# Kernel tuning notes

Hardware: AMD Instinct MI355X
Metric: run time of the kernel (lower is better)

Reference implementation:

```python
import jax, jax.numpy as jnp
import numpy as np

UNITS = 1024
NEG_INF = -10000.0


def setup_inputs() -> dict:
    key = jax.random.key(0)
    ks = jax.random.split(key, 5)
    B, S, D = 8, 2048, 1024
    scale = 0.02  # truncated-normal stddev in original init
    x = jax.random.normal(ks[0], (B, S, D), dtype=jnp.float32)
    mask = jax.random.randint(ks[1], (B, S), 0, 2, dtype=jnp.int32)
    Wq = jax.random.normal(ks[2], (D, UNITS), dtype=jnp.float32) * scale
    Wk = jax.random.normal(ks[3], (D, UNITS), dtype=jnp.float32) * scale
    Wv = jax.random.normal(ks[4], (D, UNITS), dtype=jnp.float32) * scale
    bq = jnp.zeros((UNITS,), jnp.float32)
    bk = jnp.zeros((UNITS,), jnp.float32)
    bv = jnp.zeros((UNITS,), jnp.float32)
    return {"x": x, "mask": mask, "Wq": Wq, "bq": bq, "Wk": Wk, "bk": bk, "Wv": Wv, "bv": bv}


def reference(x, mask, Wq, bq, Wk, bk, Wv, bv):
    # Q/K/V projections: [B,S,D] @ [D,U] -> [B,S,U]
    q = jnp.einsum('bsd,du->bsu', x, Wq) + bq
    k = jnp.einsum('bsd,du->bsu', x, Wk) + bk
    v = jnp.einsum('bsd,du->bsu', x, Wv) + bv
    # scaled dot-product scores: [B,S,S]
    scores = jnp.einsum('bqu,bku->bqk', q, k) / jnp.sqrt(jnp.float32(UNITS))
    m = mask.astype(jnp.float32)
    attn_mask = jnp.einsum('bq,bk->bqk', m, m)  # outer-product padding mask
    scores = scores + (1.0 - attn_mask) * NEG_INF
    probs = jax.nn.softmax(scores, axis=-1)
    # dropout is inactive at inference (training=None/False in Keras)
    context = jnp.einsum('bqk,bku->bqu', probs, v)
    return context
```

## Files before the change

### kernel.cpp

```cpp
#include <hip/hip_runtime.h>
#include <stdint.h>

typedef unsigned short u16;
typedef __bf16 bf16x8 __attribute__((ext_vector_type(8)));
typedef float f32x4 __attribute__((ext_vector_type(4)));
typedef unsigned short u16x8 __attribute__((ext_vector_type(8)));
typedef unsigned short u16x4 __attribute__((ext_vector_type(4)));

#define B_BATCH 8
#define S_LEN   2048
#define D_DIM   1024
#define U_DIM   1024

#define BK 64
#define HALF_U16  16384
#define TILE_U16  32768
#define LDS_U16   65536

__device__ __forceinline__ float bf2f(u16 h) {
    union { unsigned u; float f; } c; c.u = ((unsigned)h) << 16; return c.f;
}
__device__ __forceinline__ u16 f2bf(float f) {
    union { float f; unsigned u; } c; c.f = f;
    unsigned r = c.u + 0x7fffu + ((c.u >> 16) & 1u);
    return (u16)(r >> 16);
}

__device__ __forceinline__ void cp16(u16* lds, const u16* g) {
    __builtin_amdgcn_global_load_lds((__attribute__((address_space(1))) void*)g,
                                     (__attribute__((address_space(3))) void*)lds,
                                     16, 0, 0);
}

__device__ __forceinline__ void barrier_raw() { asm volatile("s_barrier" ::: "memory"); }

__device__ __forceinline__ void stage4(u16* __restrict__ dst, const u16* __restrict__ src,
                                       int ld, int row0, int kc, int tid) {
    #pragma unroll
    for (int s = 0; s < 4; ++s) {
        const int c = tid + 512 * s;
        const int r = c >> 3;
        const int q = (c & 7) ^ (r & 7);
        cp16(dst + c * 8, src + (long long)(row0 + r) * ld + kc + q * 8);
    }
}

__device__ __forceinline__ void ldsA8(bf16x8* a, const u16* __restrict__ T,
                                      int rbase, int lm, int lq, int sw) {
    #pragma unroll
    for (int i = 0; i < 4; ++i)
        #pragma unroll
        for (int ks = 0; ks < 2; ++ks)
            a[i * 2 + ks] = *(const bf16x8*)(T + (rbase + i * 16 + lm) * BK + (((ks * 4 + lq) ^ sw) * 8));
}
__device__ __forceinline__ void ldsB4(bf16x8* b, const u16* __restrict__ T,
                                      int rbase, int lm, int lq, int sw) {
    #pragma unroll
    for (int j = 0; j < 2; ++j)
        #pragma unroll
        for (int ks = 0; ks < 2; ++ks)
            b[j * 2 + ks] = *(const bf16x8*)(T + (rbase + j * 16 + lm) * BK + (((ks * 4 + lq) ^ sw) * 8));
}

template<int I0, int J0>
__device__ __forceinline__ void mmaq(f32x4 (*acc)[4], const bf16x8* a, const bf16x8* b) {
    __builtin_amdgcn_s_setprio(1);
    #pragma unroll
    for (int i = 0; i < 4; ++i)
        #pragma unroll
        for (int j = 0; j < 2; ++j)
            #pragma unroll
            for (int ks = 0; ks < 2; ++ks)
                acc[I0 + i][J0 + j] = __builtin_amdgcn_mfma_f32_16x16x32_bf16(
                    a[i * 2 + ks], b[j * 2 + ks], acc[I0 + i][J0 + j], 0, 0, 0);
    __builtin_amdgcn_s_setprio(0);
    __builtin_amdgcn_sched_barrier(0);
}

__device__ __forceinline__ void gemm256(
    const u16* __restrict__ A, int lda,
    const u16* __restrict__ Bt, int ldb,
    int m0, int n0, int K,
    u16* lds, int tid, f32x4 (*acc)[4])
{
    const int lane = tid & 63;
    const int wid  = tid >> 6;
    const int wmh  = (wid >> 2) * 128;
    const int wnh  = (wid & 3) * 64;
    const int lm   = lane & 15;
    const int lq   = lane >> 4;
    const int sw   = lm & 7;

    stage4(lds,            A,  lda, m0, 0, tid);
    stage4(lds + HALF_U16, Bt, ldb, n0, 0, tid);
    asm volatile("s_waitcnt vmcnt(0)" ::: "memory");
    barrier_raw();

    const int NT = K >> 6;
    int buf = 0;
    for (int kt = 0; kt < NT; ++kt) {
        const u16* As  = lds + buf * TILE_U16;
        const u16* Bs  = As + HALF_U16;
        u16* Asn = lds + (buf ^ 1) * TILE_U16;
        u16* Bsn = Asn + HALF_U16;
        const int kn = (kt + 1) << 6;
        const bool pre = (kt + 1) < NT;
        bf16x8 a[8], b[4];

        ldsA8(a, As, wmh, lm, lq, sw);
        ldsB4(b, Bs, wnh, lm, lq, sw);
        if (pre) stage4(Asn, A, lda, m0, kn, tid);
        barrier_raw();
        mmaq<0, 0>(acc, a, b);
        barrier_raw();

        ldsB4(b, Bs, wnh + 32, lm, lq, sw);
        if (pre) stage4(Bsn, Bt, ldb, n0, kn, tid);
        barrier_raw();
        mmaq<0, 2>(acc, a, b);
        barrier_raw();

        ldsA8(a, As, wmh + 64, lm, lq, sw);
        barrier_raw();
        mmaq<4, 2>(acc, a, b);
        barrier_raw();

        ldsB4(b, Bs, wnh, lm, lq, sw);
        if (pre) asm volatile("s_waitcnt vmcnt(0)" ::: "memory");
        barrier_raw();
        mmaq<4, 0>(acc, a, b);
        barrier_raw();

        buf ^= 1;
    }
}

__device__ __forceinline__ void swizzle_mnz(int ph, int& mi, int& ni, int& z) {
    const int lid = blockIdx.x + gridDim.x * (blockIdx.y + gridDim.y * blockIdx.z);
    z = lid & 7;
    const int t = lid >> 3;
    const int ntn = gridDim.x;
    const int panel = t / (ph * ntn);
    const int r = t - panel * (ph * ntn);
    mi = panel * ph + (r % ph);
    ni = r / ph;
}

__global__ __launch_bounds__(256) void prep(
    const float* __restrict__ x, u16* __restrict__ xb,
    const float* __restrict__ Wq, const float* __restrict__ Wk,
    const float* __restrict__ Wv, u16* __restrict__ WT,
    float* __restrict__ rowsum)
{
    __shared__ u16 tile[32][33];
    const int b = blockIdx.x;
    const int tid = threadIdx.x;
    if (b < 16384) {
        const int i = b * 256 + tid;
        float4 v = ((const float4*)x)[i];
        ushort4 o;
        o.x = f2bf(v.x); o.y = f2bf(v.y); o.z = f2bf(v.z); o.w = f2bf(v.w);
        ((ushort4*)xb)[i] = o;
    } else if (b < 16384 + 3072) {
        const int b2 = b - 16384;
        const int w = b2 >> 10;
        const int idx = b2 & 1023;
        const float* src = (w == 0) ? Wq : (w == 1) ? Wk : Wv;
        u16* dst = WT + (size_t)w * D_DIM * U_DIM;
        const int c0 = (idx & 31) * 32, rr0 = (idx >> 5) * 32;
        const int tx = tid & 31, ty = tid >> 5;
        #pragma unroll
        for (int i = 0; i < 32; i += 8)
            tile[ty + i][tx] = f2bf(src[(long long)(rr0 + ty + i) * U_DIM + c0 + tx]);
        __syncthreads();
        #pragma unroll
        for (int i = 0; i < 32; i += 8)
            dst[(long long)(c0 + ty + i) * D_DIM + rr0 + tx] = tile[tx][ty + i];
    } else {
        const int i = (b - 16384 - 3072) * 256 + tid;
        float4 z4; z4.x = z4.y = z4.z = z4.w = 0.0f;
        ((float4*)rowsum)[i] = z4;
    }
}

__global__ __launch_bounds__(512, 2) void qkv_proj(
    const u16* __restrict__ xb, const u16* __restrict__ WT,
    const float* __restrict__ bq, const float* __restrict__ bk,
    const float* __restrict__ bv,
    u16* __restrict__ Q, u16* __restrict__ Ko, u16* __restrict__ VT)
{
    __shared__ __align__(16) u16 smem[LDS_U16];
    const int tgt = blockIdx.x >> 2;
    const int n0 = (blockIdx.x & 3) * 256;
    const int m0 = blockIdx.y * 256;
    const int tid = threadIdx.x;
    const int lane = tid & 63, wid = tid >> 6;
    const int wmh = (wid >> 2) * 128, wnh = (wid & 3) * 64;
    const int lm = lane & 15, lq = lane >> 4;

    const u16* Bt = WT + (size_t)tgt * (D_DIM * U_DIM);
    const float* bias = (tgt == 0) ? bq : (tgt == 1) ? bk : bv;

    f32x4 acc[8][4] = {};
    gemm256(xb, D_DIM, Bt, D_DIM, m0, n0, D_DIM, smem, tid, acc);

    if (tgt < 2) {
        u16* C = (tgt == 0) ? Q : Ko;
        #pragma unroll
        for (int j = 0; j < 4; ++j) {
            const int n = n0 + wnh + j * 16 + lm;
            const float bvv = bias[n];
            #pragma unroll
            for (int i = 0; i < 8; ++i) {
                const long long mr = m0 + wmh + i * 16 + lq * 4;
                #pragma unroll
                for (int r = 0; r < 4; ++r)
                    C[(mr + r) * U_DIM + n] = f2bf(acc[i][j][r] + bvv);
            }
        }
    } else {
        __syncthreads();
        #pragma unroll
        for (int j = 0; j < 4; ++j) {
            const int cl = wnh + j * 16 + lm;
            const float bvv = bias[n0 + cl];
            #pragma unroll
            for (int i = 0; i < 8; ++i) {
                const int rowb = wmh + i * 16 + lq * 4;
                u16x4 pk;
                #pragma unroll
                for (int r = 0; r < 4; ++r) pk[r] = f2bf(acc[i][j][r] + bvv);
                const int idx = cl * 256 + (((rowb >> 3) ^ (cl & 31)) * 8) + (rowb & 7);
                *(u16x4*)(smem + idx) = pk;
            }
        }
        __syncthreads();
        const int zb = m0 >> 11;
        const int s0 = m0 & 2047;
        u16* VTg = VT + (size_t)zb * ((size_t)S_LEN * U_DIM);
        #pragma unroll
        for (int s = 0; s < 16; ++s) {
            const int cid = tid + 512 * s;
            const int cl = cid >> 5;
            const int m8 = cid & 31;
            u16x8 v = *(const u16x8*)(smem + cl * 256 + ((m8 ^ (cl & 31)) * 8));
            *(u16x8*)(VTg + (size_t)(n0 + cl) * S_LEN + s0 + m8 * 8) = v;
        }
    }
}

__global__ __launch_bounds__(512, 2) void scores_exp(
    const u16* __restrict__ Qb, const u16* __restrict__ Kb,
    u16* __restrict__ E, const int* __restrict__ mask,
    float* __restrict__ rowsum, int ph)
{
    __shared__ __align__(16) u16 smem[LDS_U16];

    int mi, ni, z;
    swizzle_mnz(ph, mi, ni, z);
    const int m0 = mi * 256, n0 = ni * 256;
    const long long SU = (long long)S_LEN * U_DIM;
    const long long SS = (long long)S_LEN * S_LEN;

    const int tid = threadIdx.x;
    const int lane = tid & 63, wid = tid >> 6;
    const int wmh = (wid >> 2) * 128, wnh = (wid & 3) * 64;
    const int lm = lane & 15, lq = lane >> 4;

    f32x4 acc[8][4] = {};
    gemm256(Qb + (long long)z * SU, U_DIM, Kb + (long long)z * SU, U_DIM,
            m0, n0, U_DIM, smem, tid, acc);

    u16* Eg = E + (long long)z * SS;
    const int* mrow = mask + (size_t)z * S_LEN;

    int mj[4];
    #pragma unroll
    for (int j = 0; j < 4; ++j) mj[j] = mrow[n0 + wnh + j * 16 + lm];

    #pragma unroll
    for (int i = 0; i < 8; ++i) {
        #pragma unroll
        for (int r = 0; r < 4; ++r) {
            const int row = m0 + wmh + i * 16 + lq * 4 + r;
            const int mi_ = mrow[row];
            float partial = 0.0f;
            #pragma unroll
            for (int j = 0; j < 4; ++j) {
                float e = (mi_ && !mj[j]) ? 0.0f : __expf(acc[i][j][r] * 0.03125f);
                const u16 h = f2bf(e);
                Eg[(long long)row * S_LEN + n0 + wnh + j * 16 + lm] = h;
                partial += bf2f(h);
            }
            partial += __shfl_xor(partial, 1, 64);
            partial += __shfl_xor(partial, 2, 64);
            partial += __shfl_xor(partial, 4, 64);
            partial += __shfl_xor(partial, 8, 64);
            if (lm == 0)
                atomicAdd(&rowsum[(size_t)z * S_LEN + row], partial);
        }
    }
}

__global__ __launch_bounds__(512, 2) void pv_gemm(
    const u16* __restrict__ E, const u16* __restrict__ VT,
    float* __restrict__ out, const float* __restrict__ rowsum, int ph)
{
    __shared__ __align__(16) u16 smem[LDS_U16];

    int mi, ni, z;
    swizzle_mnz(ph, mi, ni, z);
    const int m0 = mi * 256, n0 = ni * 256;
    const long long SU = (long long)S_LEN * U_DIM;
    const long long SS = (long long)S_LEN * S_LEN;

    const int tid = threadIdx.x;
    const int lane = tid & 63, wid = tid >> 6;
    const int wmh = (wid >> 2) * 128, wnh = (wid & 3) * 64;
    const int lm = lane & 15, lq = lane >> 4;

    f32x4 acc[8][4] = {};
    gemm256(E + (long long)z * SS, S_LEN, VT + (long long)z * SU, S_LEN,
            m0, n0, S_LEN, smem, tid, acc);

    float* Cg = out + (long long)z * SU;
    const float* rs = rowsum + (size_t)z * S_LEN;

    #pragma unroll
    for (int i = 0; i < 8; ++i) {
        #pragma unroll
        for (int r = 0; r < 4; ++r) {
            const int row = m0 + wmh + i * 16 + lq * 4 + r;
            const float inv = 1.0f / rs[row];
            #pragma unroll
            for (int j = 0; j < 4; ++j)
                Cg[(long long)row * U_DIM + n0 + wnh + j * 16 + lm] = acc[i][j][r] * inv;
        }
    }
}

extern "C" void kernel_launch(void* const* d_in, const int* in_sizes, int n_in,
                              void* d_out, int out_size, void* d_ws, size_t ws_size,
                              hipStream_t stream)
{
    (void)in_sizes; (void)n_in; (void)out_size; (void)ws_size;
    const float* x    = (const float*)d_in[0];
    const int*   mask = (const int*)d_in[1];
    const float* Wq   = (const float*)d_in[2];
    const float* bq   = (const float*)d_in[3];
    const float* Wk   = (const float*)d_in[4];
    const float* bk   = (const float*)d_in[5];
    const float* Wv   = (const float*)d_in[6];
    const float* bv   = (const float*)d_in[7];

    const size_t DU  = (size_t)D_DIM * U_DIM;
    const size_t BSU = (size_t)B_BATCH * S_LEN * U_DIM;

    u16* ws  = (u16*)d_ws;
    u16* Qb  = ws;
    u16* Kb  = Qb + BSU;
    u16* VTb = Kb + BSU;
    u16* WT  = VTb + BSU;
    float* rowsum = (float*)(WT + 3 * DU);
    u16* E   = (u16*)(rowsum + (size_t)B_BATCH * S_LEN);
    u16* xb  = E;

    prep<<<dim3(16384 + 3072 + 16), dim3(256), 0, stream>>>(x, xb, Wq, Wk, Wv, WT, rowsum);

    qkv_proj<<<dim3(12, 64), dim3(512), 0, stream>>>(xb, WT, bq, bk, bv, Qb, Kb, VTb);

    scores_exp<<<dim3(8, 8, 8), dim3(512), 0, stream>>>(Qb, Kb, E, mask, rowsum, 8);

    pv_gemm<<<dim3(4, 8, 8), dim3(512), 0, stream>>>(E, VTb, (float*)d_out, rowsum, 8);
}
```

Before: 290.1 us.

## Split GEMM K-tiles into 32-wide sub-stages with deeper staggered prefetch pipeline

Restructures the 256x256 bf16 GEMM main loop so each 64-wide K tile is stored as two 32-wide LDS sub-tiles (A and B separately) with a new XOR swizzle. Global-to-LDS copies for the next half-tiles are issued up to two sub-steps ahead, using partial vmcnt waits instead of draining to zero. The aim is to hide global load latency better and keep more MFMAs in flight between barriers. It adds explicit lgkmcnt waits and more careful counter bookkeeping, which risks stalls or ordering hazards if the vmcnt counts are off.

```diff
diff --git a/kernel.cpp b/kernel.cpp
--- a/kernel.cpp
+++ b/kernel.cpp
@@ -12,8 +12,7 @@
 #define D_DIM   1024
 #define U_DIM   1024
 
-#define BK 64
-#define HALF_U16  16384
+#define KSUB_U16  8192
 #define TILE_U16  32768
 #define LDS_U16   65536
 
@@ -34,45 +33,30 @@
 
 __device__ __forceinline__ void barrier_raw() { asm volatile("s_barrier" ::: "memory"); }
 
-__device__ __forceinline__ void stage4(u16* __restrict__ dst, const u16* __restrict__ src,
-                                       int ld, int row0, int kc, int tid) {
-    #pragma unroll
-    for (int s = 0; s < 4; ++s) {
+__device__ __forceinline__ void stg2(u16* __restrict__ dst, const u16* __restrict__ src,
+                                     int ld, int row0, int kbase, int tid) {
+    #pragma unroll
+    for (int s = 0; s < 2; ++s) {
         const int c = tid + 512 * s;
-        const int r = c >> 3;
-        const int q = (c & 7) ^ (r & 7);
-        cp16(dst + c * 8, src + (long long)(row0 + r) * ld + kc + q * 8);
-    }
-}
-
-__device__ __forceinline__ void ldsA8(bf16x8* a, const u16* __restrict__ T,
-                                      int rbase, int lm, int lq, int sw) {
+        const int r = c >> 2;
+        const int q = (c & 3) ^ ((r >> 1) & 3);
+        cp16(dst + c * 8, src + (long long)(row0 + r) * ld + kbase + q * 8);
+    }
+}
+
+__device__ __forceinline__ bf16x8 rdfrag(const u16* __restrict__ base, int row, int lq) {
+    return *(const bf16x8*)(base + row * 32 + ((lq ^ ((row >> 1) & 3)) * 8));
+}
+
+template<int I0>
+__device__ __forceinline__ void mma16(f32x4 (*acc)[4], const bf16x8* a, const bf16x8* b) {
+    __builtin_amdgcn_s_setprio(1);
     #pragma unroll
     for (int i = 0; i < 4; ++i)
         #pragma unroll
-        for (int ks = 0; ks < 2; ++ks)
-            a[i * 2 + ks] = *(const bf16x8*)(T + (rbase + i * 16 + lm) * BK + (((ks * 4 + lq) ^ sw) * 8));
-}
-__device__ __forceinline__ void ldsB4(bf16x8* b, const u16* __restrict__ T,
-                                      int rbase, int lm, int lq, int sw) {
-    #pragma unroll
-    for (int j = 0; j < 2; ++j)
-        #pragma unroll
-        for (int ks = 0; ks < 2; ++ks)
-            b[j * 2 + ks] = *(const bf16x8*)(T + (rbase + j * 16 + lm) * BK + (((ks * 4 + lq) ^ sw) * 8));
-}
-
-template<int I0, int J0>
-__device__ __forceinline__ void mmaq(f32x4 (*acc)[4], const bf16x8* a, const bf16x8* b) {
-    __builtin_amdgcn_s_setprio(1);
-    #pragma unroll
-    for (int i = 0; i < 4; ++i)
-        #pragma unroll
-        for (int j = 0; j < 2; ++j)
-            #pragma unroll
-            for (int ks = 0; ks < 2; ++ks)
-                acc[I0 + i][J0 + j] = __builtin_amdgcn_mfma_f32_16x16x32_bf16(
-                    a[i * 2 + ks], b[j * 2 + ks], acc[I0 + i][J0 + j], 0, 0, 0);
+        for (int j = 0; j < 4; ++j)
+            acc[I0 + i][j] = __builtin_amdgcn_mfma_f32_16x16x32_bf16(
+                a[i], b[j], acc[I0 + i][j], 0, 0, 0);
     __builtin_amdgcn_s_setprio(0);
     __builtin_amdgcn_sched_barrier(0);
 }
@@ -89,49 +73,77 @@
     const int wnh  = (wid & 3) * 64;
     const int lm   = lane & 15;
     const int lq   = lane >> 4;
-    const int sw   = lm & 7;
-
-    stage4(lds,            A,  lda, m0, 0, tid);
-    stage4(lds + HALF_U16, Bt, ldb, n0, 0, tid);
-    asm volatile("s_waitcnt vmcnt(0)" ::: "memory");
+    const int NT   = K >> 6;
+
+    stg2(lds + 0 * KSUB_U16, A,  lda, m0, 0,  tid);
+    stg2(lds + 1 * KSUB_U16, Bt, ldb, n0, 0,  tid);
+    stg2(lds + 2 * KSUB_U16, A,  lda, m0, 32, tid);
+    stg2(lds + 3 * KSUB_U16, Bt, ldb, n0, 32, tid);
+    if (NT > 1) {
+        stg2(lds + TILE_U16 + 0 * KSUB_U16, A,  lda, m0, 64, tid);
+        stg2(lds + TILE_U16 + 1 * KSUB_U16, Bt, ldb, n0, 64, tid);
+        asm volatile("s_waitcnt vmcnt(8)" ::: "memory");
+    } else {
+        asm volatile("s_waitcnt vmcnt(4)" ::: "memory");
+    }
     barrier_raw();
 
-    const int NT = K >> 6;
-    int buf = 0;
-    for (int kt = 0; kt < NT; ++kt) {
-        const u16* As  = lds + buf * TILE_U16;
-        const u16* Bs  = As + HALF_U16;
-        u16* Asn = lds + (buf ^ 1) * TILE_U16;
-        u16* Bsn = Asn + HALF_U16;
-        const int kn = (kt + 1) << 6;
-        const bool pre = (kt + 1) < NT;
-        bf16x8 a[8], b[4];
-
-        ldsA8(a, As, wmh, lm, lq, sw);
-        ldsB4(b, Bs, wnh, lm, lq, sw);
-        if (pre) stage4(Asn, A, lda, m0, kn, tid);
-        barrier_raw();
-        mmaq<0, 0>(acc, a, b);
-        barrier_raw();
-
-        ldsB4(b, Bs, wnh + 32, lm, lq, sw);
-        if (pre) stage4(Bsn, Bt, ldb, n0, kn, tid);
-        barrier_raw();
-        mmaq<0, 2>(acc, a, b);
-        barrier_raw();
-
-        ldsA8(a, As, wmh + 64, lm, lq, sw);
-        barrier_raw();
-        mmaq<4, 2>(acc, a, b);
-        barrier_raw();
-
-        ldsB4(b, Bs, wnh, lm, lq, sw);
-        if (pre) asm volatile("s_waitcnt vmcnt(0)" ::: "memory");
-        barrier_raw();
-        mmaq<4, 0>(acc, a, b);
-        barrier_raw();
-
-        buf ^= 1;
+    for (int t = 0; t < NT; ++t) {
+        const int s = t & 1;
+        const u16* A0b = lds + s * TILE_U16;
+        const u16* B0b = A0b + KSUB_U16;
+        const u16* A1b = A0b + 2 * KSUB_U16;
+        const u16* B1b = A0b + 3 * KSUB_U16;
+        u16* ns = lds + (s ^ 1) * TILE_U16;
+        u16* cs = lds + s * TILE_U16;
+        const bool p1 = (t + 1) < NT;
+        const bool p2 = (t + 2) < NT;
+        const int k1 = (t + 1) << 6, k2 = (t + 2) << 6;
+        bf16x8 a[4], b[4];
+
+        #pragma unroll
+        for (int i = 0; i < 4; ++i) a[i] = rdfrag(A0b, wmh + i * 16 + lm, lq);
+        #pragma unroll
+        for (int j = 0; j < 4; ++j) b[j] = rdfrag(B0b, wnh + j * 16 + lm, lq);
+        if (p1) stg2(ns + 2 * KSUB_U16, A, lda, m0, k1 + 32, tid);
+        barrier_raw();
+        asm volatile("s_waitcnt lgkmcnt(0)" ::: "memory");
+        __builtin_amdgcn_sched_barrier(0);
+        mma16<0>(acc, a, b);
+        barrier_raw();
+
+        #pragma unroll
+        for (int i = 0; i < 4; ++i) a[i] = rdfrag(A0b, wmh + 64 + i * 16 + lm, lq);
+        if (p1) stg2(ns + 3 * KSUB_U16, Bt, ldb, n0, k1 + 32, tid);
+        barrier_raw();
+        asm volatile("s_waitcnt lgkmcnt(0)" ::: "memory");
+        __builtin_amdgcn_sched_barrier(0);
+        mma16<4>(acc, a, b);
+        if (p1) asm volatile("s_waitcnt vmcnt(8)" ::: "memory");
+        else    asm volatile("s_waitcnt vmcnt(0)" ::: "memory");
+        barrier_raw();
+
+        #pragma unroll
+        for (int i = 0; i < 4; ++i) a[i] = rdfrag(A1b, wmh + i * 16 + lm, lq);
+        #pragma unroll
+        for (int j = 0; j < 4; ++j) b[j] = rdfrag(B1b, wnh + j * 16 + lm, lq);
+        if (p2) stg2(cs + 0 * KSUB_U16, A, lda, m0, k2, tid);
+        barrier_raw();
+        asm volatile("s_waitcnt lgkmcnt(0)" ::: "memory");
+        __builtin_amdgcn_sched_barrier(0);
+        mma16<0>(acc, a, b);
+        barrier_raw();
+
+        #pragma unroll
+        for (int i = 0; i < 4; ++i) a[i] = rdfrag(A1b, wmh + 64 + i * 16 + lm, lq);
+        if (p2) stg2(cs + 1 * KSUB_U16, Bt, ldb, n0, k2, tid);
+        barrier_raw();
+        asm volatile("s_waitcnt lgkmcnt(0)" ::: "memory");
+        __builtin_amdgcn_sched_barrier(0);
+        mma16<4>(acc, a, b);
+        if (p2) asm volatile("s_waitcnt vmcnt(8)" ::: "memory");
+        else    asm volatile("s_waitcnt vmcnt(0)" ::: "memory");
+        barrier_raw();
     }
 }
 
```

Result: slower. 296.1 us (+2.1%).
